# Kernel tuning notes

Measured on AMD Instinct MI355X. Metric: run time of the kernel, lower is better.

## Reference

```python
import jax, jax.numpy as jnp
import numpy as np

B, T, C, E, K, CAP, H = 8, 2048, 1024, 8, 2, 4096, 4096


def setup_inputs() -> dict:
    key = jax.random.key(0)
    ks = jax.random.split(key, 6)
    s = 0.02
    return {
        "x": jax.random.normal(ks[0], (B, T, C), jnp.float32),
        "rw1": s * jax.random.normal(ks[1], (C, H), jnp.float32),
        "rb1": jnp.zeros((H,), jnp.float32),
        "rw2": s * jax.random.normal(ks[2], (H, E), jnp.float32),
        "rb2": jnp.zeros((E,), jnp.float32),
        "ew1": s * jax.random.normal(ks[3], (E, C, H), jnp.float32),
        "eb1": jnp.zeros((E, H), jnp.float32),
        "ew2": s * jax.random.normal(ks[4], (E, H, C), jnp.float32),
        "eb2": jnp.zeros((E, C), jnp.float32),
    }


def reference(x, rw1, rb1, rw2, rb2, ew1, eb1, ew2, eb2):
    Bx, Tx, Cx = x.shape
    N = Bx * Tx
    # Router FFN -> gating logits [B,T,E]
    logits = jax.nn.relu(x @ rw1 + rb1) @ rw2 + rb2
    vals, ids = jax.lax.top_k(logits, K)           # [B,T,K]
    probs = jax.nn.softmax(vals, axis=-1)          # [B,T,K]

    ids_f = ids.reshape(N * K)                     # expert id per (token, k) slot
    probs_f = probs.reshape(N * K)
    xr = jnp.repeat(x.reshape(N, Cx), K, axis=0)   # [N*K, C], token order preserved

    # position of each slot within its expert's capacity buffer
    m = jax.nn.one_hot(ids_f, E, dtype=jnp.int32)  # [N*K, E]
    pos = jnp.cumsum(m, axis=0) - 1
    pos_tok = jnp.take_along_axis(pos, ids_f[:, None], axis=1)[:, 0]
    keep = (pos_tok < CAP).astype(x.dtype)         # drop tokens over capacity (padding)
    pos_c = jnp.clip(pos_tok, 0, CAP - 1)

    # dispatch: scatter tokens into per-expert padded buffers [E, CAP, C]
    disp = jnp.zeros((E, CAP, Cx), x.dtype).at[ids_f, pos_c].add(xr * keep[:, None])

    # expert FFN, batched over experts
    h = jax.nn.relu(jnp.einsum('enc,ech->enh', disp, ew1) + eb1[:, None, :])
    eo = jnp.einsum('enh,ehc->enc', h, ew2) + eb2[:, None, :]

    # combine: gather expert outputs back, weight by gate prob, sum over k
    y = eo[ids_f, pos_c] * (probs_f * keep)[:, None]   # [N*K, C]
    return y.reshape(Bx, Tx, K, Cx).sum(axis=2)
```

## Files before the change

### kernel.cpp

```cpp
#include <hip/hip_runtime.h>
#include <cstdint>
#include <type_traits>

#define B_    8
#define T_    2048
#define C_    1024
#define E_    8
#define K_    2
#define CAP_  4096
#define H_    4096
#define NTOK  (B_ * T_)
#define NSLOT (NTOK * K_)
#define KR_   3072

typedef __bf16 bf16x8 __attribute__((ext_vector_type(8)));
typedef float  f32x4  __attribute__((ext_vector_type(4)));

#define AS1 __attribute__((address_space(1)))
#define AS3 __attribute__((address_space(3)))

static __device__ __forceinline__ float b2f(unsigned short u) {
    union { float f; unsigned int i; } v; v.i = ((unsigned int)u) << 16; return v.f;
}
static __device__ __forceinline__ unsigned short f2b(float f) {
    unsigned int x = __float_as_uint(f);
    unsigned int r = (x + 0x7fffu + ((x >> 16) & 1u)) >> 16;
    return (unsigned short)r;
}

template<int W> static __device__ __forceinline__ void vm_wait() {
    if constexpr (W == 4) asm volatile("s_waitcnt vmcnt(4)" ::: "memory");
    else if constexpr (W == 0) asm volatile("s_waitcnt vmcnt(0)" ::: "memory");
}

template<int RELU, typename TC>
__global__ __launch_bounds__(512, 2) void gemm256_8ph(
    const unsigned short* __restrict__ A, const unsigned short* __restrict__ BT,
    const float* __restrict__ bias, TC* __restrict__ Cout,
    int Kd, int Nld, int NT,
    long sA, long sB, long sBias, long sC)
{
    extern __shared__ char smem[];

    const int z = blockIdx.z;
    A    += (size_t)z * sA;
    BT   += (size_t)z * sB;
    bias += (size_t)z * sBias;
    Cout += (size_t)z * sC;

    const int gx = gridDim.x;
    const int nwg = gx * gridDim.y;
    int wg = blockIdx.y * gx + blockIdx.x;
    wg = (wg & 7) * (nwg >> 3) + (wg >> 3);
    const int bm = (wg / gx) * 256;
    const int bn = (wg % gx) * 256;

    const int tid  = threadIdx.x;
    const int lane = tid & 63;
    const int wid  = tid >> 6;
    const int wrow = (wid >> 2) * 128;
    const int wcol = (wid & 3) * 64;
    const int fr = lane & 15;
    const int fq = lane >> 4;

    const size_t rbA = (size_t)Kd * 2;
    const char* Ag = (const char*)A  + (size_t)bm * rbA;
    const char* Bg = (const char*)BT + (size_t)bn * rbA;

    f32x4 acc[8][4];
#pragma unroll
    for (int i = 0; i < 8; i++)
#pragma unroll
        for (int j = 0; j < 4; j++) acc[i][j] = (f32x4){0.f, 0.f, 0.f, 0.f};

    auto STAGE_A = [&](int kt) {
        char* d = smem + (size_t)(kt & 1) * 65536;
        const size_t kb = (size_t)kt * 128;
#pragma unroll
        for (int r = 0; r < 4; ++r) {
            const int o    = r * 8192 + tid * 16;
            const int row  = o >> 7;
            const int slot = (o >> 4) & 7;
            const int ss   = (slot ^ (row & 7)) << 4;
            __builtin_amdgcn_global_load_lds(
                (const AS1 void*)(Ag + (size_t)row * rbA + kb + ss),
                (AS3 void*)(d + r * 8192 + wid * 1024), 16, 0, 0);
        }
    };
    auto STAGE_B = [&](int kt) {
        char* d = smem + (size_t)(kt & 1) * 65536 + 32768;
        const size_t kb = (size_t)kt * 128;
#pragma unroll
        for (int r = 0; r < 4; ++r) {
            const int o    = r * 8192 + tid * 16;
            const int row  = o >> 7;
            const int slot = (o >> 4) & 7;
            const int ss   = (slot ^ (row & 7)) << 4;
            __builtin_amdgcn_global_load_lds(
                (const AS1 void*)(Bg + (size_t)row * rbA + kb + ss),
                (AS3 void*)(d + r * 8192 + wid * 1024), 16, 0, 0);
        }
    };

    auto LDA = [&](int kt, int mi, int kk) -> bf16x8 {
        const char* base = smem + (size_t)(kt & 1) * 65536;
        const int row  = wrow + mi * 16 + fr;
        const int slot = (kk * 4 + fq) ^ (row & 7);
        return *(const bf16x8*)(base + row * 128 + slot * 16);
    };
    auto LDB = [&](int kt, int ni, int kk) -> bf16x8 {
        const char* base = smem + (size_t)(kt & 1) * 65536 + 32768;
        const int row  = wcol + ni * 16 + fr;
        const int slot = (kk * 4 + fq) ^ (row & 7);
        return *(const bf16x8*)(base + row * 128 + slot * 16);
    };

    STAGE_A(0); STAGE_B(0); STAGE_B(1);
    vm_wait<4>();
    __builtin_amdgcn_s_barrier();

    bf16x8 a[4], bb[4];
    for (int kt = 0; kt < NT; ++kt) {
#pragma unroll
        for (int i = 0; i < 4; ++i) a[i]  = LDA(kt, i, 0);
#pragma unroll
        for (int i = 0; i < 4; ++i) bb[i] = LDB(kt, i, 0);
        if (kt + 1 < NT) STAGE_A(kt + 1);
        __builtin_amdgcn_s_barrier();
        __builtin_amdgcn_s_setprio(1);
#pragma unroll
        for (int mi = 0; mi < 4; ++mi)
#pragma unroll
            for (int ni = 0; ni < 4; ++ni)
                acc[mi][ni] = __builtin_amdgcn_mfma_f32_16x16x32_bf16(
                    a[mi], bb[ni], acc[mi][ni], 0, 0, 0);
        __builtin_amdgcn_s_setprio(0);
        __builtin_amdgcn_s_barrier();
#pragma unroll
        for (int i = 0; i < 4; ++i) a[i] = LDA(kt, 4 + i, 0);
        __builtin_amdgcn_s_barrier();
        __builtin_amdgcn_s_setprio(1);
#pragma unroll
        for (int mi = 0; mi < 4; ++mi)
#pragma unroll
            for (int ni = 0; ni < 4; ++ni)
                acc[4 + mi][ni] = __builtin_amdgcn_mfma_f32_16x16x32_bf16(
                    a[mi], bb[ni], acc[4 + mi][ni], 0, 0, 0);
        __builtin_amdgcn_s_setprio(0);
        __builtin_amdgcn_s_barrier();
#pragma unroll
        for (int i = 0; i < 4; ++i) a[i]  = LDA(kt, i, 1);
#pragma unroll
        for (int i = 0; i < 4; ++i) bb[i] = LDB(kt, i, 1);
        __builtin_amdgcn_s_barrier();
        __builtin_amdgcn_s_setprio(1);
#pragma unroll
        for (int mi = 0; mi < 4; ++mi)
#pragma unroll
            for (int ni = 0; ni < 4; ++ni)
                acc[mi][ni] = __builtin_amdgcn_mfma_f32_16x16x32_bf16(
                    a[mi], bb[ni], acc[mi][ni], 0, 0, 0);
        __builtin_amdgcn_s_setprio(0);
        __builtin_amdgcn_s_barrier();
#pragma unroll
        for (int i = 0; i < 4; ++i) a[i] = LDA(kt, 4 + i, 1);
        if (kt + 2 < NT) STAGE_B(kt + 2);
        if (kt + 1 < NT) {
            if (kt + 2 < NT) vm_wait<4>();
            else             vm_wait<0>();
        }
        __builtin_amdgcn_s_barrier();
        __builtin_amdgcn_s_setprio(1);
#pragma unroll
        for (int mi = 0; mi < 4; ++mi)
#pragma unroll
            for (int ni = 0; ni < 4; ++ni)
                acc[4 + mi][ni] = __builtin_amdgcn_mfma_f32_16x16x32_bf16(
                    a[mi], bb[ni], acc[4 + mi][ni], 0, 0, 0);
        __builtin_amdgcn_s_setprio(0);
        __builtin_amdgcn_s_barrier();
    }

    const float* bias_o = bias;
    asm volatile("" : "+s"(bias_o));
#pragma unroll
    for (int mi = 0; mi < 8; ++mi) {
#pragma unroll
        for (int ni = 0; ni < 4; ++ni) {
            const int c = bn + wcol + ni * 16 + fr;
            const float bv = bias_o[c];
#pragma unroll
            for (int rg = 0; rg < 4; ++rg) {
                const int r = bm + wrow + mi * 16 + fq * 4 + rg;
                float v = acc[mi][ni][rg] + bv;
                if (RELU) v = fmaxf(v, 0.f);
                if constexpr (std::is_same_v<TC, float>)
                    Cout[(size_t)r * Nld + c] = v;
                else
                    Cout[(size_t)r * Nld + c] = f2b(v);
            }
        }
    }
}

__global__ __launch_bounds__(256) void split_x(
    const float* __restrict__ x, unsigned short* __restrict__ A2)
{
    const int n = blockIdx.x;
    const int c = threadIdx.x * 4;
    const float4 v = *(const float4*)(x + (size_t)n * C_ + c);
    ushort4 hi, lo;
    hi.x = f2b(v.x); lo.x = f2b(v.x - b2f(hi.x));
    hi.y = f2b(v.y); lo.y = f2b(v.y - b2f(hi.y));
    hi.z = f2b(v.z); lo.z = f2b(v.z - b2f(hi.z));
    hi.w = f2b(v.w); lo.w = f2b(v.w - b2f(hi.w));
    unsigned short* row = A2 + (size_t)n * KR_;
    *(ushort4*)(row + c)            = hi;
    *(ushort4*)(row + C_ + c)       = lo;
    *(ushort4*)(row + 2 * C_ + c)   = hi;
}

__global__ __launch_bounds__(256) void split_w(
    const float* __restrict__ in, unsigned short* __restrict__ out)
{
    __shared__ float t[32][33];
    const int rb = blockIdx.y * 32;
    const int cb = blockIdx.x * 32;
    const int tr = threadIdx.x >> 3, tc = (threadIdx.x & 7) * 4;
    const float4 v = *(const float4*)(in + (size_t)(rb + tr) * H_ + cb + tc);
    t[tr][tc + 0] = v.x; t[tr][tc + 1] = v.y; t[tr][tc + 2] = v.z; t[tr][tc + 3] = v.w;
    __syncthreads();
    ushort4 hi, lo;
    float f;
    f = t[tc + 0][tr]; hi.x = f2b(f); lo.x = f2b(f - b2f(hi.x));
    f = t[tc + 1][tr]; hi.y = f2b(f); lo.y = f2b(f - b2f(hi.y));
    f = t[tc + 2][tr]; hi.z = f2b(f); lo.z = f2b(f - b2f(hi.z));
    f = t[tc + 3][tr]; hi.w = f2b(f); lo.w = f2b(f - b2f(hi.w));
    unsigned short* row = out + (size_t)(cb + tr) * KR_;
    *(ushort4*)(row + rb + tc)           = hi;
    *(ushort4*)(row + C_ + rb + tc)      = hi;
    *(ushort4*)(row + 2 * C_ + rb + tc)  = lo;
}

__global__ __launch_bounds__(256) void transpose_cvt(
    const float* __restrict__ in, unsigned short* __restrict__ out, int R, int Ncols)
{
    __shared__ float t[32][33];
    const size_t zoff = (size_t)blockIdx.z * R * Ncols;
    in  += zoff;
    out += zoff;
    const int rb = blockIdx.y * 32, cb = blockIdx.x * 32;
    const int tr = threadIdx.x >> 3, tc = (threadIdx.x & 7) * 4;
    const float4 v = *(const float4*)(in + (size_t)(rb + tr) * Ncols + cb + tc);
    t[tr][tc + 0] = v.x; t[tr][tc + 1] = v.y; t[tr][tc + 2] = v.z; t[tr][tc + 3] = v.w;
    __syncthreads();
    ushort4 u;
    u.x = f2b(t[tc + 0][tr]); u.y = f2b(t[tc + 1][tr]);
    u.z = f2b(t[tc + 2][tr]); u.w = f2b(t[tc + 3][tr]);
    *(ushort4*)(out + (size_t)(cb + tr) * R + rb + tc) = u;
}

__global__ __launch_bounds__(256) void router_topk(
    const float* __restrict__ h1, const float* __restrict__ rw2,
    const float* __restrict__ rb2, int* __restrict__ ids, float* __restrict__ probs)
{
    const int n = blockIdx.x;
    const float* hrow = h1 + (size_t)n * H_;
    float acc[E_];
#pragma unroll
    for (int e = 0; e < E_; e++) acc[e] = 0.f;
    for (int h = threadIdx.x; h < H_; h += 256) {
        const float hv = hrow[h];
        const float4 w0 = *(const float4*)(rw2 + (size_t)h * E_);
        const float4 w1 = *(const float4*)(rw2 + (size_t)h * E_ + 4);
        acc[0] = fmaf(hv, w0.x, acc[0]); acc[1] = fmaf(hv, w0.y, acc[1]);
        acc[2] = fmaf(hv, w0.z, acc[2]); acc[3] = fmaf(hv, w0.w, acc[3]);
        acc[4] = fmaf(hv, w1.x, acc[4]); acc[5] = fmaf(hv, w1.y, acc[5]);
        acc[6] = fmaf(hv, w1.z, acc[6]); acc[7] = fmaf(hv, w1.w, acc[7]);
    }
    __shared__ float red[E_][256];
#pragma unroll
    for (int e = 0; e < E_; e++) red[e][threadIdx.x] = acc[e];
    __syncthreads();
    for (int st = 128; st > 0; st >>= 1) {
        if (threadIdx.x < st) {
#pragma unroll
            for (int e = 0; e < E_; e++) red[e][threadIdx.x] += red[e][threadIdx.x + st];
        }
        __syncthreads();
    }
    if (threadIdx.x == 0) {
        float v1 = -1e30f, v2 = -1e30f; int i1 = 0, i2 = 0;
#pragma unroll
        for (int e = 0; e < E_; e++) {
            const float v = red[e][0] + rb2[e];
            if (v > v1)      { v2 = v1; i2 = i1; v1 = v; i1 = e; }
            else if (v > v2) { v2 = v;  i2 = e; }
        }
        const float e2 = expf(v2 - v1);
        const float inv = 1.f / (1.f + e2);
        ids[n * 2] = i1;  ids[n * 2 + 1] = i2;
        probs[n * 2] = inv; probs[n * 2 + 1] = e2 * inv;
    }
}

__global__ __launch_bounds__(256) void compute_pos(
    const int* __restrict__ ids, int* __restrict__ pos)
{
    __shared__ int hist[256][E_];
    const int t = threadIdx.x;
    const int per = NSLOT / 256;
    int cnt[E_];
#pragma unroll
    for (int e = 0; e < E_; e++) cnt[e] = 0;
    const int s0 = t * per;
    for (int i = 0; i < per; i++) cnt[ids[s0 + i]]++;
#pragma unroll
    for (int e = 0; e < E_; e++) hist[t][e] = cnt[e];
    __syncthreads();
    if (t < E_) {
        int run = 0;
        for (int i = 0; i < 256; i++) { const int c = hist[i][t]; hist[i][t] = run; run += c; }
    }
    __syncthreads();
    int run[E_];
#pragma unroll
    for (int e = 0; e < E_; e++) run[e] = hist[t][e];
    for (int i = 0; i < per; i++) { const int e = ids[s0 + i]; pos[s0 + i] = run[e]++; }
}

__global__ __launch_bounds__(256) void dispatch_k(
    const float* __restrict__ x, const int* __restrict__ ids,
    const int* __restrict__ pos, unsigned short* __restrict__ disp)
{
    const int s = blockIdx.x;
    const int e = ids[s], p = pos[s];
    if (p >= CAP_) return;
    const int n = s >> 1;
    const float4 v = *(const float4*)(x + (size_t)n * C_ + threadIdx.x * 4);
    ushort4 u;
    u.x = f2b(v.x); u.y = f2b(v.y); u.z = f2b(v.z); u.w = f2b(v.w);
    *(ushort4*)(disp + ((size_t)e * CAP_ + p) * C_ + threadIdx.x * 4) = u;
}

__global__ __launch_bounds__(256) void combine_k(
    const unsigned short* __restrict__ eo, const int* __restrict__ ids,
    const int* __restrict__ pos, const float* __restrict__ probs,
    float* __restrict__ y)
{
    const int n = blockIdx.x;
    const int c = threadIdx.x * 4;
    float r0 = 0.f, r1 = 0.f, r2 = 0.f, r3 = 0.f;
#pragma unroll
    for (int k = 0; k < K_; k++) {
        const int p = pos[2 * n + k];
        if (p >= CAP_) continue;
        const int e = ids[2 * n + k];
        const float w = probs[2 * n + k];
        const ushort4 u = *(const ushort4*)(eo + ((size_t)e * CAP_ + p) * C_ + c);
        r0 = fmaf(w, b2f(u.x), r0); r1 = fmaf(w, b2f(u.y), r1);
        r2 = fmaf(w, b2f(u.z), r2); r3 = fmaf(w, b2f(u.w), r3);
    }
    *(float4*)(y + (size_t)n * C_ + c) = make_float4(r0, r1, r2, r3);
}

extern "C" void kernel_launch(void* const* d_in, const int* in_sizes, int n_in,
                              void* d_out, int out_size, void* d_ws, size_t ws_size,
                              hipStream_t stream)
{
    const float* x   = (const float*)d_in[0];
    const float* rw1 = (const float*)d_in[1];
    const float* rb1 = (const float*)d_in[2];
    const float* rw2 = (const float*)d_in[3];
    const float* rb2 = (const float*)d_in[4];
    const float* ew1 = (const float*)d_in[5];
    const float* eb1 = (const float*)d_in[6];
    const float* ew2 = (const float*)d_in[7];
    const float* eb2 = (const float*)d_in[8];
    float* y = (float*)d_out;

    char* ws = (char*)d_ws;
    float*          h1    = (float*)ws;
    unsigned short* hexp  = (unsigned short*)ws;
    unsigned short* A2    = (unsigned short*)(ws + 268435456L);
    unsigned short* B2    = (unsigned short*)(ws + 369098752L);
    unsigned short* disp  = (unsigned short*)(ws + 268435456L);
    unsigned short* eo    = (unsigned short*)(ws + 268435456L);
    unsigned short* BTW   = (unsigned short*)(ws + 335544320L);
    int*            ids   = (int*)  (ws + 402653184L);
    float*          probs = (float*)(ws + 402784256L);
    int*            pos   = (int*)  (ws + 402915328L);

    const size_t LDSB = 131072;

    split_x<<<NTOK, 256, 0, stream>>>(x, A2);
    {
        dim3 g(H_ / 32, C_ / 32, 1);
        split_w<<<g, 256, 0, stream>>>(rw1, B2);
    }
    {
        dim3 g(H_ / 256, NTOK / 256, 1);
        gemm256_8ph<1, float><<<g, 512, LDSB, stream>>>(
            A2, B2, rb1, h1, KR_, H_, KR_ / 64, 0, 0, 0, 0);
    }
    router_topk<<<NTOK, 256, 0, stream>>>(h1, rw2, rb2, ids, probs);
    compute_pos<<<1, 256, 0, stream>>>(ids, pos);
    dispatch_k<<<NSLOT, 256, 0, stream>>>(x, ids, pos, disp);
    {
        dim3 g(H_ / 32, C_ / 32, E_);
        transpose_cvt<<<g, 256, 0, stream>>>(ew1, BTW, C_, H_);
    }
    {
        dim3 g(H_ / 256, CAP_ / 256, E_);
        gemm256_8ph<1, unsigned short><<<g, 512, LDSB, stream>>>(
            disp, BTW, eb1, hexp, C_, H_, C_ / 64,
            (long)CAP_ * C_, (long)H_ * C_, (long)H_, (long)CAP_ * H_);
    }
    {
        dim3 g(C_ / 32, H_ / 32, E_);
        transpose_cvt<<<g, 256, 0, stream>>>(ew2, BTW, H_, C_);
    }
    {
        dim3 g(C_ / 256, CAP_ / 256, E_);
        gemm256_8ph<0, unsigned short><<<g, 512, LDSB, stream>>>(
            hexp, BTW, eb2, eo, H_, C_, H_ / 64,
            (long)CAP_ * H_, (long)C_ * H_, (long)C_, (long)CAP_ * C_);
    }
    combine_k<<<NTOK, 256, 0, stream>>>(eo, ids, pos, probs, y);
}
```

Baseline: 1.202 ms.

## Software-pipeline LDS fragment loads one MFMA phase ahead with separate register sets

Splits the A/B fragment registers into distinct per-phase sets so each LDS read for the next MFMA block is issued before the current block's MFMAs run, including prefetching the next k-tile's first fragments at the end of the iteration. Scheduling barriers pin the load and compute order. The intent is to hide LDS read latency behind matrix-core work instead of stalling at each phase. It costs extra VGPRs for the additional fragment arrays, which could reduce occupancy or cause spills.

```diff
diff --git a/kernel.cpp b/kernel.cpp
--- a/kernel.cpp
+++ b/kernel.cpp
@@ -119,13 +119,17 @@
     vm_wait<4>();
     __builtin_amdgcn_s_barrier();
 
-    bf16x8 a[4], bb[4];
+    bf16x8 aA[4], aB[4], aC[4], aD[4], bbA[4], bbB[4];
+#pragma unroll
+    for (int i = 0; i < 4; ++i) aA[i]  = LDA(0, i, 0);
+#pragma unroll
+    for (int i = 0; i < 4; ++i) bbA[i] = LDB(0, i, 0);
+
     for (int kt = 0; kt < NT; ++kt) {
 #pragma unroll
-        for (int i = 0; i < 4; ++i) a[i]  = LDA(kt, i, 0);
-#pragma unroll
-        for (int i = 0; i < 4; ++i) bb[i] = LDB(kt, i, 0);
+        for (int i = 0; i < 4; ++i) aB[i] = LDA(kt, 4 + i, 0);
         if (kt + 1 < NT) STAGE_A(kt + 1);
+        __builtin_amdgcn_sched_barrier(0);
         __builtin_amdgcn_s_barrier();
         __builtin_amdgcn_s_setprio(1);
 #pragma unroll
@@ -133,11 +137,14 @@
 #pragma unroll
             for (int ni = 0; ni < 4; ++ni)
                 acc[mi][ni] = __builtin_amdgcn_mfma_f32_16x16x32_bf16(
-                    a[mi], bb[ni], acc[mi][ni], 0, 0, 0);
+                    aA[mi], bbA[ni], acc[mi][ni], 0, 0, 0);
         __builtin_amdgcn_s_setprio(0);
         __builtin_amdgcn_s_barrier();
 #pragma unroll
-        for (int i = 0; i < 4; ++i) a[i] = LDA(kt, 4 + i, 0);
+        for (int i = 0; i < 4; ++i) aC[i]  = LDA(kt, i, 1);
+#pragma unroll
+        for (int i = 0; i < 4; ++i) bbB[i] = LDB(kt, i, 1);
+        __builtin_amdgcn_sched_barrier(0);
         __builtin_amdgcn_s_barrier();
         __builtin_amdgcn_s_setprio(1);
 #pragma unroll
@@ -145,13 +152,12 @@
 #pragma unroll
             for (int ni = 0; ni < 4; ++ni)
                 acc[4 + mi][ni] = __builtin_amdgcn_mfma_f32_16x16x32_bf16(
-                    a[mi], bb[ni], acc[4 + mi][ni], 0, 0, 0);
+                    aB[mi], bbA[ni], acc[4 + mi][ni], 0, 0, 0);
         __builtin_amdgcn_s_setprio(0);
         __builtin_amdgcn_s_barrier();
 #pragma unroll
-        for (int i = 0; i < 4; ++i) a[i]  = LDA(kt, i, 1);
-#pragma unroll
-        for (int i = 0; i < 4; ++i) bb[i] = LDB(kt, i, 1);
+        for (int i = 0; i < 4; ++i) aD[i] = LDA(kt, 4 + i, 1);
+        __builtin_amdgcn_sched_barrier(0);
         __builtin_amdgcn_s_barrier();
         __builtin_amdgcn_s_setprio(1);
 #pragma unroll
@@ -159,24 +165,25 @@
 #pragma unroll
             for (int ni = 0; ni < 4; ++ni)
                 acc[mi][ni] = __builtin_amdgcn_mfma_f32_16x16x32_bf16(
-                    a[mi], bb[ni], acc[mi][ni], 0, 0, 0);
+                    aC[mi], bbB[ni], acc[mi][ni], 0, 0, 0);
         __builtin_amdgcn_s_setprio(0);
         __builtin_amdgcn_s_barrier();
-#pragma unroll
-        for (int i = 0; i < 4; ++i) a[i] = LDA(kt, 4 + i, 1);
-        if (kt + 2 < NT) STAGE_B(kt + 2);
+        if (kt + 2 < NT) { STAGE_B(kt + 2); vm_wait<4>(); }
+        else if (kt + 1 < NT) vm_wait<0>();
+        __builtin_amdgcn_s_barrier();
         if (kt + 1 < NT) {
-            if (kt + 2 < NT) vm_wait<4>();
-            else             vm_wait<0>();
-        }
-        __builtin_amdgcn_s_barrier();
+#pragma unroll
+            for (int i = 0; i < 4; ++i) aA[i]  = LDA(kt + 1, i, 0);
+#pragma unroll
+            for (int i = 0; i < 4; ++i) bbA[i] = LDB(kt + 1, i, 0);
+        }
         __builtin_amdgcn_s_setprio(1);
 #pragma unroll
         for (int mi = 0; mi < 4; ++mi)
 #pragma unroll
             for (int ni = 0; ni < 4; ++ni)
                 acc[4 + mi][ni] = __builtin_amdgcn_mfma_f32_16x16x32_bf16(
-                    a[mi], bb[ni], acc[4 + mi][ni], 0, 0, 0);
+                    aD[mi], bbB[ni], acc[4 + mi][ni], 0, 0, 0);
         __builtin_amdgcn_s_setprio(0);
         __builtin_amdgcn_s_barrier();
     }
```

After: 1.216 ms. About the same (+1.2%).

## Run router GEMM in fp16 and recompute only near-tie tokens precisely

Applied to the files above, without the earlier changes.

The router's first layer now runs as a single fp16 GEMM over K=1024 instead of the three-pass bf16 split GEMM. Tokens whose top-3 logit gaps fall under a margin are collected into a list. Only those rows are re-split and recomputed with the precise GEMM, and the results are scattered back before the router top-k is redone. This cuts most of the router GEMM work, at the cost of extra kernels, atomics and a data-dependent recompute whose size depends on how many tokens are near ties.

```diff
diff --git a/kernel.cpp b/kernel.cpp
--- a/kernel.cpp
+++ b/kernel.cpp
@@ -12,9 +12,11 @@
 #define NTOK  (B_ * T_)
 #define NSLOT (NTOK * K_)
 #define KR_   3072
-
-typedef __bf16 bf16x8 __attribute__((ext_vector_type(8)));
-typedef float  f32x4  __attribute__((ext_vector_type(4)));
+#define MARGIN_ 8e-3f
+
+typedef __bf16    bf16x8 __attribute__((ext_vector_type(8)));
+typedef _Float16  half8  __attribute__((ext_vector_type(8)));
+typedef float     f32x4  __attribute__((ext_vector_type(4)));
 
 #define AS1 __attribute__((address_space(1)))
 #define AS3 __attribute__((address_space(3)))
@@ -27,18 +29,23 @@
     unsigned int r = (x + 0x7fffu + ((x >> 16) & 1u)) >> 16;
     return (unsigned short)r;
 }
+static __device__ __forceinline__ unsigned short f2h(float f) {
+    _Float16 h = (_Float16)f;
+    return __builtin_bit_cast(unsigned short, h);
+}
 
 template<int W> static __device__ __forceinline__ void vm_wait() {
     if constexpr (W == 4) asm volatile("s_waitcnt vmcnt(4)" ::: "memory");
     else if constexpr (W == 0) asm volatile("s_waitcnt vmcnt(0)" ::: "memory");
 }
 
-template<int RELU, typename TC>
+template<int RELU, typename TC, bool F16, bool SCAT>
 __global__ __launch_bounds__(512, 2) void gemm256_8ph(
     const unsigned short* __restrict__ A, const unsigned short* __restrict__ BT,
     const float* __restrict__ bias, TC* __restrict__ Cout,
     int Kd, int Nld, int NT,
-    long sA, long sB, long sBias, long sC)
+    long sA, long sB, long sBias, long sC,
+    const int* __restrict__ lst, const int* __restrict__ cnt)
 {
     extern __shared__ char smem[];
 
@@ -54,6 +61,12 @@
     wg = (wg & 7) * (nwg >> 3) + (wg >> 3);
     const int bm = (wg / gx) * 256;
     const int bn = (wg % gx) * 256;
+
+    int nf = 0;
+    if constexpr (SCAT) {
+        nf = *cnt;
+        if (bm >= nf) return;
+    }
 
     const int tid  = threadIdx.x;
     const int lane = tid & 63;
@@ -114,6 +127,13 @@
         const int slot = (kk * 4 + fq) ^ (row & 7);
         return *(const bf16x8*)(base + row * 128 + slot * 16);
     };
+    auto MFMA = [&](f32x4 c, bf16x8 a, bf16x8 b) -> f32x4 {
+        if constexpr (F16)
+            return __builtin_amdgcn_mfma_f32_16x16x32_f16(
+                __builtin_bit_cast(half8, a), __builtin_bit_cast(half8, b), c, 0, 0, 0);
+        else
+            return __builtin_amdgcn_mfma_f32_16x16x32_bf16(a, b, c, 0, 0, 0);
+    };
 
     STAGE_A(0); STAGE_B(0); STAGE_B(1);
     vm_wait<4>();
@@ -132,8 +152,7 @@
         for (int mi = 0; mi < 4; ++mi)
 #pragma unroll
             for (int ni = 0; ni < 4; ++ni)
-                acc[mi][ni] = __builtin_amdgcn_mfma_f32_16x16x32_bf16(
-                    a[mi], bb[ni], acc[mi][ni], 0, 0, 0);
+                acc[mi][ni] = MFMA(acc[mi][ni], a[mi], bb[ni]);
         __builtin_amdgcn_s_setprio(0);
         __builtin_amdgcn_s_barrier();
 #pragma unroll
@@ -144,8 +163,7 @@
         for (int mi = 0; mi < 4; ++mi)
 #pragma unroll
             for (int ni = 0; ni < 4; ++ni)
-                acc[4 + mi][ni] = __builtin_amdgcn_mfma_f32_16x16x32_bf16(
-                    a[mi], bb[ni], acc[4 + mi][ni], 0, 0, 0);
+                acc[4 + mi][ni] = MFMA(acc[4 + mi][ni], a[mi], bb[ni]);
         __builtin_amdgcn_s_setprio(0);
         __builtin_amdgcn_s_barrier();
 #pragma unroll
@@ -158,8 +176,7 @@
         for (int mi = 0; mi < 4; ++mi)
 #pragma unroll
             for (int ni = 0; ni < 4; ++ni)
-                acc[mi][ni] = __builtin_amdgcn_mfma_f32_16x16x32_bf16(
-                    a[mi], bb[ni], acc[mi][ni], 0, 0, 0);
+                acc[mi][ni] = MFMA(acc[mi][ni], a[mi], bb[ni]);
         __builtin_amdgcn_s_setprio(0);
         __builtin_amdgcn_s_barrier();
 #pragma unroll
@@ -175,8 +192,7 @@
         for (int mi = 0; mi < 4; ++mi)
 #pragma unroll
             for (int ni = 0; ni < 4; ++ni)
-                acc[4 + mi][ni] = __builtin_amdgcn_mfma_f32_16x16x32_bf16(
-                    a[mi], bb[ni], acc[4 + mi][ni], 0, 0, 0);
+                acc[4 + mi][ni] = MFMA(acc[4 + mi][ni], a[mi], bb[ni]);
         __builtin_amdgcn_s_setprio(0);
         __builtin_amdgcn_s_barrier();
     }
@@ -194,19 +210,39 @@
                 const int r = bm + wrow + mi * 16 + fq * 4 + rg;
                 float v = acc[mi][ni][rg] + bv;
                 if (RELU) v = fmaxf(v, 0.f);
-                if constexpr (std::is_same_v<TC, float>)
+                if constexpr (SCAT) {
+                    if (r < nf) {
+                        const int t = lst[r];
+                        ((float*)Cout)[(size_t)t * Nld + c] = v;
+                    }
+                } else if constexpr (std::is_same_v<TC, float>) {
                     Cout[(size_t)r * Nld + c] = v;
-                else
+                } else {
                     Cout[(size_t)r * Nld + c] = f2b(v);
+                }
             }
         }
     }
 }
 
-__global__ __launch_bounds__(256) void split_x(
-    const float* __restrict__ x, unsigned short* __restrict__ A2)
+__global__ __launch_bounds__(256) void split_x16(
+    const float* __restrict__ x, unsigned short* __restrict__ x16)
 {
     const int n = blockIdx.x;
+    const int c = threadIdx.x * 4;
+    const float4 v = *(const float4*)(x + (size_t)n * C_ + c);
+    ushort4 u;
+    u.x = f2h(v.x); u.y = f2h(v.y); u.z = f2h(v.z); u.w = f2h(v.w);
+    *(ushort4*)(x16 + (size_t)n * C_ + c) = u;
+}
+
+__global__ __launch_bounds__(256) void gather_split(
+    const float* __restrict__ x, const int* __restrict__ list,
+    const int* __restrict__ count, unsigned short* __restrict__ Axc)
+{
+    const int i = blockIdx.x;
+    if (i >= *count) return;
+    const int n = list[i];
     const int c = threadIdx.x * 4;
     const float4 v = *(const float4*)(x + (size_t)n * C_ + c);
     ushort4 hi, lo;
@@ -214,10 +250,10 @@
     hi.y = f2b(v.y); lo.y = f2b(v.y - b2f(hi.y));
     hi.z = f2b(v.z); lo.z = f2b(v.z - b2f(hi.z));
     hi.w = f2b(v.w); lo.w = f2b(v.w - b2f(hi.w));
-    unsigned short* row = A2 + (size_t)n * KR_;
-    *(ushort4*)(row + c)            = hi;
-    *(ushort4*)(row + C_ + c)       = lo;
-    *(ushort4*)(row + 2 * C_ + c)   = hi;
+    unsigned short* row = Axc + (size_t)i * KR_;
+    *(ushort4*)(row + c)          = hi;
+    *(ushort4*)(row + C_ + c)     = lo;
+    *(ushort4*)(row + 2 * C_ + c) = hi;
 }
 
 __global__ __launch_bounds__(256) void split_w(
@@ -242,6 +278,7 @@
     *(ushort4*)(row + 2 * C_ + rb + tc)  = lo;
 }
 
+template<bool H16>
 __global__ __launch_bounds__(256) void transpose_cvt(
     const float* __restrict__ in, unsigned short* __restrict__ out, int R, int Ncols)
 {
@@ -255,16 +292,24 @@
     t[tr][tc + 0] = v.x; t[tr][tc + 1] = v.y; t[tr][tc + 2] = v.z; t[tr][tc + 3] = v.w;
     __syncthreads();
     ushort4 u;
-    u.x = f2b(t[tc + 0][tr]); u.y = f2b(t[tc + 1][tr]);
-    u.z = f2b(t[tc + 2][tr]); u.w = f2b(t[tc + 3][tr]);
+    if constexpr (H16) {
+        u.x = f2h(t[tc + 0][tr]); u.y = f2h(t[tc + 1][tr]);
+        u.z = f2h(t[tc + 2][tr]); u.w = f2h(t[tc + 3][tr]);
+    } else {
+        u.x = f2b(t[tc + 0][tr]); u.y = f2b(t[tc + 1][tr]);
+        u.z = f2b(t[tc + 2][tr]); u.w = f2b(t[tc + 3][tr]);
+    }
     *(ushort4*)(out + (size_t)(cb + tr) * R + rb + tc) = u;
 }
 
-__global__ __launch_bounds__(256) void router_topk(
+template<int MODE>
+__global__ __launch_bounds__(256) void router_topk_m(
     const float* __restrict__ h1, const float* __restrict__ rw2,
-    const float* __restrict__ rb2, int* __restrict__ ids, float* __restrict__ probs)
+    const float* __restrict__ rb2, int* __restrict__ ids, float* __restrict__ probs,
+    int* __restrict__ flagv, int* __restrict__ list, int* __restrict__ count)
 {
     const int n = blockIdx.x;
+    if (MODE == 1 && !flagv[n]) return;
     const float* hrow = h1 + (size_t)n * H_;
     float acc[E_];
 #pragma unroll
@@ -290,17 +335,25 @@
         __syncthreads();
     }
     if (threadIdx.x == 0) {
-        float v1 = -1e30f, v2 = -1e30f; int i1 = 0, i2 = 0;
+        float v1 = -1e30f, v2 = -1e30f, v3 = -1e30f; int i1 = 0, i2 = 0;
 #pragma unroll
         for (int e = 0; e < E_; e++) {
             const float v = red[e][0] + rb2[e];
-            if (v > v1)      { v2 = v1; i2 = i1; v1 = v; i1 = e; }
-            else if (v > v2) { v2 = v;  i2 = e; }
+            if (v > v1)      { v3 = v2; v2 = v1; i2 = i1; v1 = v; i1 = e; }
+            else if (v > v2) { v3 = v2; v2 = v;  i2 = e; }
+            else if (v > v3) { v3 = v; }
         }
         const float e2 = expf(v2 - v1);
         const float inv = 1.f / (1.f + e2);
         ids[n * 2] = i1;  ids[n * 2 + 1] = i2;
         probs[n * 2] = inv; probs[n * 2 + 1] = e2 * inv;
+        if (MODE == 0) {
+            if ((v1 - v2 < MARGIN_) || (v2 - v3 < MARGIN_)) {
+                flagv[n] = 1;
+                const int idx = atomicAdd(count, 1);
+                list[idx] = n;
+            }
+        }
     }
 }
 
@@ -382,49 +435,72 @@
     char* ws = (char*)d_ws;
     float*          h1    = (float*)ws;
     unsigned short* hexp  = (unsigned short*)ws;
-    unsigned short* A2    = (unsigned short*)(ws + 268435456L);
-    unsigned short* B2    = (unsigned short*)(ws + 369098752L);
+    unsigned short* W16T  = (unsigned short*)(ws + 268435456L);
+    unsigned short* Axc   = (unsigned short*)(ws + 268435456L);
     unsigned short* disp  = (unsigned short*)(ws + 268435456L);
     unsigned short* eo    = (unsigned short*)(ws + 268435456L);
     unsigned short* BTW   = (unsigned short*)(ws + 335544320L);
+    unsigned short* B2    = (unsigned short*)(ws + 369098752L);
+    unsigned short* x16   = (unsigned short*)(ws + 369098752L);
     int*            ids   = (int*)  (ws + 402653184L);
     float*          probs = (float*)(ws + 402784256L);
     int*            pos   = (int*)  (ws + 402915328L);
+    int*            flagv = (int*)  (ws + 403046400L);
+    int*            list  = (int*)  (ws + 403111936L);
+    int*            count = (int*)  (ws + 403177472L);
 
     const size_t LDSB = 131072;
 
-    split_x<<<NTOK, 256, 0, stream>>>(x, A2);
+    hipMemsetAsync(count, 0, 128, stream);
+    hipMemsetAsync(flagv, 0, NTOK * sizeof(int), stream);
+
+    split_x16<<<NTOK, 256, 0, stream>>>(x, x16);
+    {
+        dim3 g(H_ / 32, C_ / 32, 1);
+        transpose_cvt<true><<<g, 256, 0, stream>>>(rw1, W16T, C_, H_);
+    }
+    {
+        dim3 g(H_ / 256, NTOK / 256, 1);
+        gemm256_8ph<1, float, true, false><<<g, 512, LDSB, stream>>>(
+            x16, W16T, rb1, h1, C_, H_, C_ / 64, 0, 0, 0, 0, nullptr, nullptr);
+    }
+    router_topk_m<0><<<NTOK, 256, 0, stream>>>(h1, rw2, rb2, ids, probs,
+                                               flagv, list, count);
+    gather_split<<<NTOK, 256, 0, stream>>>(x, list, count, Axc);
     {
         dim3 g(H_ / 32, C_ / 32, 1);
         split_w<<<g, 256, 0, stream>>>(rw1, B2);
     }
     {
         dim3 g(H_ / 256, NTOK / 256, 1);
-        gemm256_8ph<1, float><<<g, 512, LDSB, stream>>>(
-            A2, B2, rb1, h1, KR_, H_, KR_ / 64, 0, 0, 0, 0);
-    }
-    router_topk<<<NTOK, 256, 0, stream>>>(h1, rw2, rb2, ids, probs);
+        gemm256_8ph<1, float, false, true><<<g, 512, LDSB, stream>>>(
+            Axc, B2, rb1, h1, KR_, H_, KR_ / 64, 0, 0, 0, 0, list, count);
+    }
+    router_topk_m<1><<<NTOK, 256, 0, stream>>>(h1, rw2, rb2, ids, probs,
+                                               flagv, list, count);
     compute_pos<<<1, 256, 0, stream>>>(ids, pos);
     dispatch_k<<<NSLOT, 256, 0, stream>>>(x, ids, pos, disp);
     {
         dim3 g(H_ / 32, C_ / 32, E_);
-        transpose_cvt<<<g, 256, 0, stream>>>(ew1, BTW, C_, H_);
+        transpose_cvt<false><<<g, 256, 0, stream>>>(ew1, BTW, C_, H_);
     }
     {
         dim3 g(H_ / 256, CAP_ / 256, E_);
-        gemm256_8ph<1, unsigned short><<<g, 512, LDSB, stream>>>(
+        gemm256_8ph<1, unsigned short, false, false><<<g, 512, LDSB, stream>>>(
             disp, BTW, eb1, hexp, C_, H_, C_ / 64,
-            (long)CAP_ * C_, (long)H_ * C_, (long)H_, (long)CAP_ * H_);
+            (long)CAP_ * C_, (long)H_ * C_, (long)H_, (long)CAP_ * H_,
+            nullptr, nullptr);
     }
     {
         dim3 g(C_ / 32, H_ / 32, E_);
-        transpose_cvt<<<g, 256, 0, stream>>>(ew2, BTW, H_, C_);
+        transpose_cvt<false><<<g, 256, 0, stream>>>(ew2, BTW, H_, C_);
     }
     {
         dim3 g(C_ / 256, CAP_ / 256, E_);
-        gemm256_8ph<0, unsigned short><<<g, 512, LDSB, stream>>>(
+        gemm256_8ph<0, unsigned short, false, false><<<g, 512, LDSB, stream>>>(
             hexp, BTW, eb2, eo, H_, C_, H_ / 64,
-            (long)CAP_ * H_, (long)C_ * H_, (long)C_, (long)CAP_ * C_);
+            (long)CAP_ * H_, (long)C_ * H_, (long)C_, (long)CAP_ * C_,
+            nullptr, nullptr);
     }
     combine_k<<<NTOK, 256, 0, stream>>>(eo, ids, pos, probs, y);
 }
```

Result: no change. 1.208 ms (+0.5%).

## Fuse router second layer into first router GEMM epilogue via partial logits

Applied to the files above, without the earlier changes.

The router GEMM epilogue now applies bias and ReLU, multiplies each tile's hidden slice by the matching rw2 rows held in LDS, and reduces across lanes and waves to per-tile partial logits. These are written to a small buffer instead of the full fp32 hidden activation. A new per-thread kernel sums the 16 partials per token and does top-2 plus softmax. This removes a 256 MB fp32 write and read-back, but changes summation order and adds LDS and shuffle work to the epilogue.

```diff
diff --git a/kernel.cpp b/kernel.cpp
--- a/kernel.cpp
+++ b/kernel.cpp
@@ -33,12 +33,13 @@
     else if constexpr (W == 0) asm volatile("s_waitcnt vmcnt(0)" ::: "memory");
 }
 
-template<int RELU, typename TC>
+template<int RELU, typename TC, int EPI>
 __global__ __launch_bounds__(512, 2) void gemm256_8ph(
     const unsigned short* __restrict__ A, const unsigned short* __restrict__ BT,
     const float* __restrict__ bias, TC* __restrict__ Cout,
     int Kd, int Nld, int NT,
-    long sA, long sB, long sBias, long sC)
+    long sA, long sB, long sBias, long sC,
+    const float* __restrict__ rw2v, float* __restrict__ plogv)
 {
     extern __shared__ char smem[];
 
@@ -46,7 +47,7 @@
     A    += (size_t)z * sA;
     BT   += (size_t)z * sB;
     bias += (size_t)z * sBias;
-    Cout += (size_t)z * sC;
+    if constexpr (EPI == 0) Cout += (size_t)z * sC;
 
     const int gx = gridDim.x;
     const int nwg = gx * gridDim.y;
@@ -183,24 +184,111 @@
 
     const float* bias_o = bias;
     asm volatile("" : "+s"(bias_o));
-#pragma unroll
-    for (int mi = 0; mi < 8; ++mi) {
-#pragma unroll
-        for (int ni = 0; ni < 4; ++ni) {
-            const int c = bn + wcol + ni * 16 + fr;
-            const float bv = bias_o[c];
+
+    if constexpr (EPI == 3) {
+        float* rw2s = (float*)smem;
+        float* pl   = (float*)(smem + 8192);
+        *(float4*)(rw2s + tid * 4) =
+            *(const float4*)(rw2v + (size_t)bn * 8 + tid * 4);
+        __syncthreads();
+
+        float bv[4];
+#pragma unroll
+        for (int ni = 0; ni < 4; ++ni)
+            bv[ni] = bias_o[bn + wcol + ni * 16 + fr];
+
+#pragma unroll
+        for (int mi = 0; mi < 8; ++mi) {
 #pragma unroll
             for (int rg = 0; rg < 4; ++rg) {
-                const int r = bm + wrow + mi * 16 + fq * 4 + rg;
-                float v = acc[mi][ni][rg] + bv;
-                if (RELU) v = fmaxf(v, 0.f);
-                if constexpr (std::is_same_v<TC, float>)
-                    Cout[(size_t)r * Nld + c] = v;
-                else
-                    Cout[(size_t)r * Nld + c] = f2b(v);
+                float p[8];
+#pragma unroll
+                for (int e = 0; e < 8; ++e) p[e] = 0.f;
+#pragma unroll
+                for (int ni = 0; ni < 4; ++ni) {
+                    const float h = fmaxf(acc[mi][ni][rg] + bv[ni], 0.f);
+                    const float* w8 = rw2s + (wcol + ni * 16 + fr) * 8;
+#pragma unroll
+                    for (int e = 0; e < 8; ++e) p[e] = fmaf(h, w8[e], p[e]);
+                }
+#pragma unroll
+                for (int e = 0; e < 8; ++e) {
+                    p[e] += __shfl_xor(p[e], 1, 16);
+                    p[e] += __shfl_xor(p[e], 2, 16);
+                    p[e] += __shfl_xor(p[e], 4, 16);
+                    p[e] += __shfl_xor(p[e], 8, 16);
+                }
+                if (fr == 0) {
+                    const int row = wrow + mi * 16 + fq * 4 + rg;
+                    float* dst = pl + ((wid & 3) * 256 + row) * 8;
+#pragma unroll
+                    for (int e = 0; e < 8; ++e) dst[e] = p[e];
+                }
             }
         }
-    }
+        __syncthreads();
+        {
+            const int idx = tid * 4;
+            const float4 s0 = *(float4*)(pl + 0 * 2048 + idx);
+            const float4 s1 = *(float4*)(pl + 1 * 2048 + idx);
+            const float4 s2 = *(float4*)(pl + 2 * 2048 + idx);
+            const float4 s3 = *(float4*)(pl + 3 * 2048 + idx);
+            float4 r;
+            r.x = ((s0.x + s1.x) + s2.x) + s3.x;
+            r.y = ((s0.y + s1.y) + s2.y) + s3.y;
+            r.z = ((s0.z + s1.z) + s2.z) + s3.z;
+            r.w = ((s0.w + s1.w) + s2.w) + s3.w;
+            const int row = idx >> 3, e0 = idx & 7;
+            *(float4*)(plogv + ((size_t)(bn >> 8) * NTOK + bm + row) * 8 + e0) = r;
+        }
+    } else {
+#pragma unroll
+        for (int mi = 0; mi < 8; ++mi) {
+#pragma unroll
+            for (int ni = 0; ni < 4; ++ni) {
+                const int c = bn + wcol + ni * 16 + fr;
+                const float bv = bias_o[c];
+#pragma unroll
+                for (int rg = 0; rg < 4; ++rg) {
+                    const int r = bm + wrow + mi * 16 + fq * 4 + rg;
+                    float v = acc[mi][ni][rg] + bv;
+                    if (RELU) v = fmaxf(v, 0.f);
+                    if constexpr (std::is_same_v<TC, float>)
+                        Cout[(size_t)r * Nld + c] = v;
+                    else
+                        Cout[(size_t)r * Nld + c] = f2b(v);
+                }
+            }
+        }
+    }
+}
+
+__global__ __launch_bounds__(256) void router_topk_final(
+    const float* __restrict__ plog, const float* __restrict__ rb2,
+    int* __restrict__ ids, float* __restrict__ probs)
+{
+    const int n = blockIdx.x * 256 + threadIdx.x;
+    float l[E_];
+#pragma unroll
+    for (int e = 0; e < E_; ++e) l[e] = rb2[e];
+#pragma unroll
+    for (int bx = 0; bx < 16; ++bx) {
+        const float4 a = *(const float4*)(plog + ((size_t)bx * NTOK + n) * 8);
+        const float4 b = *(const float4*)(plog + ((size_t)bx * NTOK + n) * 8 + 4);
+        l[0] += a.x; l[1] += a.y; l[2] += a.z; l[3] += a.w;
+        l[4] += b.x; l[5] += b.y; l[6] += b.z; l[7] += b.w;
+    }
+    float v1 = -1e30f, v2 = -1e30f; int i1 = 0, i2 = 0;
+#pragma unroll
+    for (int e = 0; e < E_; ++e) {
+        const float v = l[e];
+        if (v > v1)      { v2 = v1; i2 = i1; v1 = v; i1 = e; }
+        else if (v > v2) { v2 = v;  i2 = e; }
+    }
+    const float e2 = expf(v2 - v1);
+    const float inv = 1.f / (1.f + e2);
+    ids[n * 2] = i1;  ids[n * 2 + 1] = i2;
+    probs[n * 2] = inv; probs[n * 2 + 1] = e2 * inv;
 }
 
 __global__ __launch_bounds__(256) void split_x(
@@ -260,50 +348,6 @@
     *(ushort4*)(out + (size_t)(cb + tr) * R + rb + tc) = u;
 }
 
-__global__ __launch_bounds__(256) void router_topk(
-    const float* __restrict__ h1, const float* __restrict__ rw2,
-    const float* __restrict__ rb2, int* __restrict__ ids, float* __restrict__ probs)
-{
-    const int n = blockIdx.x;
-    const float* hrow = h1 + (size_t)n * H_;
-    float acc[E_];
-#pragma unroll
-    for (int e = 0; e < E_; e++) acc[e] = 0.f;
-    for (int h = threadIdx.x; h < H_; h += 256) {
-        const float hv = hrow[h];
-        const float4 w0 = *(const float4*)(rw2 + (size_t)h * E_);
-        const float4 w1 = *(const float4*)(rw2 + (size_t)h * E_ + 4);
-        acc[0] = fmaf(hv, w0.x, acc[0]); acc[1] = fmaf(hv, w0.y, acc[1]);
-        acc[2] = fmaf(hv, w0.z, acc[2]); acc[3] = fmaf(hv, w0.w, acc[3]);
-        acc[4] = fmaf(hv, w1.x, acc[4]); acc[5] = fmaf(hv, w1.y, acc[5]);
-        acc[6] = fmaf(hv, w1.z, acc[6]); acc[7] = fmaf(hv, w1.w, acc[7]);
-    }
-    __shared__ float red[E_][256];
-#pragma unroll
-    for (int e = 0; e < E_; e++) red[e][threadIdx.x] = acc[e];
-    __syncthreads();
-    for (int st = 128; st > 0; st >>= 1) {
-        if (threadIdx.x < st) {
-#pragma unroll
-            for (int e = 0; e < E_; e++) red[e][threadIdx.x] += red[e][threadIdx.x + st];
-        }
-        __syncthreads();
-    }
-    if (threadIdx.x == 0) {
-        float v1 = -1e30f, v2 = -1e30f; int i1 = 0, i2 = 0;
-#pragma unroll
-        for (int e = 0; e < E_; e++) {
-            const float v = red[e][0] + rb2[e];
-            if (v > v1)      { v2 = v1; i2 = i1; v1 = v; i1 = e; }
-            else if (v > v2) { v2 = v;  i2 = e; }
-        }
-        const float e2 = expf(v2 - v1);
-        const float inv = 1.f / (1.f + e2);
-        ids[n * 2] = i1;  ids[n * 2 + 1] = i2;
-        probs[n * 2] = inv; probs[n * 2 + 1] = e2 * inv;
-    }
-}
-
 __global__ __launch_bounds__(256) void compute_pos(
     const int* __restrict__ ids, int* __restrict__ pos)
 {
@@ -380,13 +424,13 @@
     float* y = (float*)d_out;
 
     char* ws = (char*)d_ws;
-    float*          h1    = (float*)ws;
     unsigned short* hexp  = (unsigned short*)ws;
     unsigned short* A2    = (unsigned short*)(ws + 268435456L);
-    unsigned short* B2    = (unsigned short*)(ws + 369098752L);
     unsigned short* disp  = (unsigned short*)(ws + 268435456L);
     unsigned short* eo    = (unsigned short*)(ws + 268435456L);
     unsigned short* BTW   = (unsigned short*)(ws + 335544320L);
+    unsigned short* B2    = (unsigned short*)(ws + 369098752L);
+    float*          plog  = (float*)(ws + 394264576L);
     int*            ids   = (int*)  (ws + 402653184L);
     float*          probs = (float*)(ws + 402784256L);
     int*            pos   = (int*)  (ws + 402915328L);
@@ -400,10 +444,11 @@
     }
     {
         dim3 g(H_ / 256, NTOK / 256, 1);
-        gemm256_8ph<1, float><<<g, 512, LDSB, stream>>>(
-            A2, B2, rb1, h1, KR_, H_, KR_ / 64, 0, 0, 0, 0);
-    }
-    router_topk<<<NTOK, 256, 0, stream>>>(h1, rw2, rb2, ids, probs);
+        gemm256_8ph<1, float, 3><<<g, 512, LDSB, stream>>>(
+            A2, B2, rb1, (float*)nullptr, KR_, H_, KR_ / 64, 0, 0, 0, 0,
+            rw2, plog);
+    }
+    router_topk_final<<<NTOK / 256, 256, 0, stream>>>(plog, rb2, ids, probs);
     compute_pos<<<1, 256, 0, stream>>>(ids, pos);
     dispatch_k<<<NSLOT, 256, 0, stream>>>(x, ids, pos, disp);
     {
@@ -412,9 +457,10 @@
     }
     {
         dim3 g(H_ / 256, CAP_ / 256, E_);
-        gemm256_8ph<1, unsigned short><<<g, 512, LDSB, stream>>>(
+        gemm256_8ph<1, unsigned short, 0><<<g, 512, LDSB, stream>>>(
             disp, BTW, eb1, hexp, C_, H_, C_ / 64,
-            (long)CAP_ * C_, (long)H_ * C_, (long)H_, (long)CAP_ * H_);
+            (long)CAP_ * C_, (long)H_ * C_, (long)H_, (long)CAP_ * H_,
+            nullptr, nullptr);
     }
     {
         dim3 g(C_ / 32, H_ / 32, E_);
@@ -422,9 +468,10 @@
     }
     {
         dim3 g(C_ / 256, CAP_ / 256, E_);
-        gemm256_8ph<0, unsigned short><<<g, 512, LDSB, stream>>>(
+        gemm256_8ph<0, unsigned short, 0><<<g, 512, LDSB, stream>>>(
             hexp, BTW, eb2, eo, H_, C_, H_ / 64,
-            (long)CAP_ * H_, (long)C_ * H_, (long)C_, (long)CAP_ * C_);
+            (long)CAP_ * H_, (long)C_ * H_, (long)C_, (long)CAP_ * C_,
+            nullptr, nullptr);
     }
     combine_k<<<NTOK, 256, 0, stream>>>(eo, ids, pos, probs, y);
 }
```

After: 1.192 ms. No clear change (-0.9%).
